# Kernel optimization log

Measured on AMD Instinct MI355X. Metric: run time of the kernel, lower is better.

Reference implementation:

```python
import jax, jax.numpy as jnp
import numpy as np

V, E = 100000, 128
B, Q, D = 512, 32, 256
K_NUM, SIGMA, EXACT_SIGMA = 21, 0.1, 0.001
EPS = 1e-8


def _kernel_params():
    # faithful to source (including the sigma/exact_sigma swap at the call site)
    l_mu = [1.0]
    bin_size = 2.0 / (K_NUM - 1)
    l_mu.append(1 - bin_size / 2)
    for j in range(1, K_NUM - 1):
        l_mu.append(l_mu[j] - bin_size)
    mus = sorted(l_mu)
    # kernel_sigmas(n, sigma=exact_sigma, exact_sigma=sigma) due to swapped call
    sig_list = [SIGMA] + [EXACT_SIGMA] * (K_NUM - 1)
    sigmas = sorted(sig_list)[::-1]
    return (jnp.asarray(mus, dtype=jnp.float32),
            jnp.asarray(sigmas, dtype=jnp.float32))

MUS, SIGMAS = _kernel_params()


def setup_inputs() -> dict:
    key = jax.random.key(0)
    ks = jax.random.split(key, 11)
    emb = jax.random.normal(ks[0], (V, E), dtype=jnp.float32)
    emb = emb.at[0].set(0.0)  # padding_idx=0
    w1 = jax.random.normal(ks[1], (K_NUM, 10), dtype=jnp.float32) / np.sqrt(K_NUM)
    b1 = jax.random.normal(ks[2], (10,), dtype=jnp.float32) * 0.01
    w2 = jax.random.normal(ks[3], (10, 5), dtype=jnp.float32) / np.sqrt(10)
    b2 = jax.random.normal(ks[4], (5,), dtype=jnp.float32) * 0.01
    w3 = jax.random.normal(ks[5], (5, 1), dtype=jnp.float32) / np.sqrt(5)
    b3 = jax.random.normal(ks[6], (1,), dtype=jnp.float32) * 0.01
    query1 = jax.random.randint(ks[7], (B, Q), 0, V, dtype=jnp.int64 if jax.config.jax_enable_x64 else jnp.int32)
    doc1 = jax.random.randint(ks[8], (B, D), 0, V, dtype=query1.dtype)
    query2 = jax.random.randint(ks[9], (B, Q), 0, V, dtype=query1.dtype)
    doc2 = jax.random.randint(ks[10], (B, D), 0, V, dtype=query1.dtype)
    return {"emb": emb, "w1": w1, "b1": b1, "w2": w2, "b2": b2,
            "w3": w3, "b3": b3, "query1": query1, "doc1": doc1,
            "query2": query2, "doc2": doc2}


def _l2norm(x):
    n = jnp.linalg.norm(x, axis=-1, keepdims=True)
    return x / jnp.maximum(n, EPS)


def _predict(emb, w1, b1, w2, b2, w3, b3, q_idx, d_idx):
    q_idx = jnp.clip(q_idx, 0, V - 1)
    d_idx = jnp.clip(d_idx, 0, V - 1)
    qn = _l2norm(emb[q_idx])            # [B,Q,E]
    dn = _l2norm(emb[d_idx])            # [B,D,E]
    mm = jnp.einsum('bqe,bde->bqd', qn, dn)  # cosine matching matrix [B,Q,D]
    # soft-histogram Gaussian kernel pooling: [B,Q,D,K]
    phi = jnp.exp(-0.5 * (mm[..., None] - MUS) ** 2 / SIGMAS ** 2)
    k_out = jnp.log1p(phi.sum(axis=2)).sum(axis=1)  # [B,K]
    x = jax.nn.relu(k_out) @ w1 + b1
    x = jax.nn.relu(x) @ w2 + b2
    x = jax.nn.relu(x) @ w3 + b3
    return x  # [B,1]


def reference(emb, w1, b1, w2, b2, w3, b3, query1, doc1, query2, doc2):
    logits_1 = _predict(emb, w1, b1, w2, b2, w3, b3, query1, doc1)
    logits_2 = _predict(emb, w1, b1, w2, b2, w3, b3, query2, doc2)
    return jax.nn.sigmoid(logits_1 - logits_2)
```

## Files before the change

### kernel.cpp

```cpp
#include <hip/hip_runtime.h>
#include <math.h>

#define V_SIZE 100000
#define E_DIM  128
#define B_SIZE 512
#define Q_LEN  32
#define D_LEN  256
#define K_NUM  21
#define ASTR   136


typedef _Float16 half8_t __attribute__((ext_vector_type(8)));
typedef float    float4_t __attribute__((ext_vector_type(4)));

__global__ __launch_bounds__(256, 4) void knrm_main(
    const float* __restrict__ emb,
    const int* __restrict__ q1, const int* __restrict__ d1,
    const int* __restrict__ q2, const int* __restrict__ d2,
    const float* __restrict__ w1, const float* __restrict__ b1,
    const float* __restrict__ w2, const float* __restrict__ b2,
    const float* __restrict__ w3, const float* __restrict__ b3,
    float* __restrict__ logits)
{
    const int b    = blockIdx.x;
    const int pair = blockIdx.y;
    const int t    = threadIdx.x;
    const int* __restrict__ qidx = pair ? q2 : q1;
    const int* __restrict__ didx = pair ? d2 : d1;

    __shared__ __align__(16) _Float16 Ah[Q_LEN * ASTR];
    __shared__ __align__(16) _Float16 Al[Q_LEN * ASTR];
    __shared__ __align__(16) _Float16 Bh[32 * ASTR];
    __shared__ __align__(16) _Float16 Bl[32 * ASTR];
    __shared__ float rnq[Q_LEN];
    __shared__ float rnd_s[32];
    __shared__ float phis[Q_LEN][22];
    __shared__ float ko[K_NUM];

    const int lane = t & 63;
    const int w    = t >> 6;
    const int quad = lane >> 4;
    const int l15  = lane & 15;
    const int qt   = w >> 1;
    const int dt   = w & 1;

    for (int i = t; i < Q_LEN * 22; i += 256) ((float*)phis)[i] = 0.f;

    const int drow = t >> 3;
    const int dcol = (t & 7) * 4;
    int dix[8];
    #pragma unroll
    for (int c = 0; c < 8; ++c) {
        int di = didx[b * D_LEN + c * 32 + drow];
        dix[c] = min(max(di, 0), V_SIZE - 1);
    }
    float4 pref[4];
    {
        const float4* dr = (const float4*)(emb + (size_t)dix[0] * E_DIM) + dcol;
        pref[0] = dr[0]; pref[1] = dr[1]; pref[2] = dr[2]; pref[3] = dr[3];
    }

    {
        const int qr = t >> 3;
        const int qc = t & 7;
        int qi = qidx[b * Q_LEN + qr];
        qi = min(max(qi, 0), V_SIZE - 1);
        const float4* src = (const float4*)(emb + (size_t)qi * E_DIM) + qc * 4;
        float4 v0 = src[0], v1 = src[1], v2 = src[2], v3 = src[3];
        float fv[16] = {v0.x,v0.y,v0.z,v0.w, v1.x,v1.y,v1.z,v1.w,
                        v2.x,v2.y,v2.z,v2.w, v3.x,v3.y,v3.z,v3.w};
        float ss = 0.f;
        half8_t h0, h1, l0, l1;
        #pragma unroll
        for (int j = 0; j < 8; ++j) {
            ss = fmaf(fv[j], fv[j], ss);
            _Float16 h = (_Float16)fv[j];
            h0[j] = h; l0[j] = (_Float16)(fv[j] - (float)h);
        }
        #pragma unroll
        for (int j = 0; j < 8; ++j) {
            ss = fmaf(fv[8 + j], fv[8 + j], ss);
            _Float16 h = (_Float16)fv[8 + j];
            h1[j] = h; l1[j] = (_Float16)(fv[8 + j] - (float)h);
        }
        *(half8_t*)&Ah[qr * ASTR + qc * 16]     = h0;
        *(half8_t*)&Ah[qr * ASTR + qc * 16 + 8] = h1;
        *(half8_t*)&Al[qr * ASTR + qc * 16]     = l0;
        *(half8_t*)&Al[qr * ASTR + qc * 16 + 8] = l1;
        ss += __shfl_xor(ss, 1, 8);
        ss += __shfl_xor(ss, 2, 8);
        ss += __shfl_xor(ss, 4, 8);
        if (qc == 0) rnq[qr] = 1.0f / fmaxf(sqrtf(ss), 1e-8f);
    }
    __syncthreads();

    float rnq4[4];
    #pragma unroll
    for (int r = 0; r < 4; ++r) rnq4[r] = rnq[qt * 16 + quad * 4 + r];

    const float cc0 = -0.5f / (0.1f * 0.1f);
    const float ccs = -0.5f / (0.001f * 0.001f);
    float breg[4] = {0.f, 0.f, 0.f, 0.f};

    for (int c = 0; c < 8; ++c) {
        {
            float fv[16] = {pref[0].x,pref[0].y,pref[0].z,pref[0].w,
                            pref[1].x,pref[1].y,pref[1].z,pref[1].w,
                            pref[2].x,pref[2].y,pref[2].z,pref[2].w,
                            pref[3].x,pref[3].y,pref[3].z,pref[3].w};
            float ss = 0.f;
            half8_t h0, h1, l0, l1;
            #pragma unroll
            for (int j = 0; j < 8; ++j) {
                ss = fmaf(fv[j], fv[j], ss);
                _Float16 h = (_Float16)fv[j];
                h0[j] = h; l0[j] = (_Float16)(fv[j] - (float)h);
            }
            #pragma unroll
            for (int j = 0; j < 8; ++j) {
                ss = fmaf(fv[8 + j], fv[8 + j], ss);
                _Float16 h = (_Float16)fv[8 + j];
                h1[j] = h; l1[j] = (_Float16)(fv[8 + j] - (float)h);
            }
            const int co = (t & 7) * 16;
            *(half8_t*)&Bh[drow * ASTR + co]     = h0;
            *(half8_t*)&Bh[drow * ASTR + co + 8] = h1;
            *(half8_t*)&Bl[drow * ASTR + co]     = l0;
            *(half8_t*)&Bl[drow * ASTR + co + 8] = l1;
            ss += __shfl_xor(ss, 1, 8);
            ss += __shfl_xor(ss, 2, 8);
            ss += __shfl_xor(ss, 4, 8);
            if ((t & 7) == 0) rnd_s[drow] = 1.0f / fmaxf(sqrtf(ss), 1e-8f);
        }
        __syncthreads();

        if (c < 7) {
            const float4* dr = (const float4*)(emb + (size_t)dix[c + 1] * E_DIM) + dcol;
            pref[0] = dr[0]; pref[1] = dr[1]; pref[2] = dr[2]; pref[3] = dr[3];
        }

        float4_t acc = {0.f, 0.f, 0.f, 0.f};
        const int arow = (qt * 16 + l15) * ASTR;
        const int brow = (dt * 16 + l15) * ASTR;
        #pragma unroll
        for (int s = 0; s < 4; ++s) {
            const int kof = s * 32 + quad * 8;
            half8_t ah = *(const half8_t*)&Ah[arow + kof];
            half8_t al = *(const half8_t*)&Al[arow + kof];
            half8_t bh = *(const half8_t*)&Bh[brow + kof];
            half8_t bl = *(const half8_t*)&Bl[brow + kof];
            acc = __builtin_amdgcn_mfma_f32_16x16x32_f16(ah, bh, acc, 0, 0, 0);
            acc = __builtin_amdgcn_mfma_f32_16x16x32_f16(ah, bl, acc, 0, 0, 0);
            acc = __builtin_amdgcn_mfma_f32_16x16x32_f16(al, bh, acc, 0, 0, 0);
        }

        const float rdv = rnd_s[dt * 16 + l15];
        #pragma unroll
        for (int r = 0; r < 4; ++r) {
            const float mm = acc[r] * rnq4[r] * rdv;
            const float x0 = mm + 0.95f;
            breg[r] += __expf(x0 * x0 * cc0);
            float g = rintf((mm + 0.85f) * 10.f);
            g = fminf(fmaxf(g, 0.f), 18.f);
            float mu = fmaf(g, 0.1f, -0.85f);
            int ks = (int)g + 1;
            if (mm > 0.975f) { mu = 1.0f; ks = 20; }
            const float xs = mm - mu;
            const float es = __expf(xs * xs * ccs);
            if (es > 0.f) atomicAdd(&phis[qt * 16 + quad * 4 + r][ks], es);
        }
        __syncthreads();
    }

    #pragma unroll
    for (int r = 0; r < 4; ++r) {
        float v = breg[r];
        v += __shfl_xor(v, 1, 16);
        v += __shfl_xor(v, 2, 16);
        v += __shfl_xor(v, 4, 16);
        v += __shfl_xor(v, 8, 16);
        if (l15 == 0) atomicAdd(&phis[qt * 16 + quad * 4 + r][0], v);
    }
    __syncthreads();

    for (int p = t; p < K_NUM * Q_LEN; p += 256) {
        const int q = p & 31;
        const int k = p >> 5;
        float l = log1pf(phis[q][k]);
        l += __shfl_xor(l, 1, 32);
        l += __shfl_xor(l, 2, 32);
        l += __shfl_xor(l, 4, 32);
        l += __shfl_xor(l, 8, 32);
        l += __shfl_xor(l, 16, 32);
        if (q == 0) ko[k] = l;
    }
    __syncthreads();

    if (t == 0) {
        float x1v[10];
        #pragma unroll
        for (int i = 0; i < 10; ++i) {
            float s = b1[i];
            for (int k = 0; k < K_NUM; ++k) {
                float v = ko[k] > 0.f ? ko[k] : 0.f;
                s = fmaf(v, w1[k * 10 + i], s);
            }
            x1v[i] = s;
        }
        float x2v[5];
        #pragma unroll
        for (int i = 0; i < 5; ++i) {
            float s = b2[i];
            #pragma unroll
            for (int k = 0; k < 10; ++k) {
                float v = x1v[k] > 0.f ? x1v[k] : 0.f;
                s = fmaf(v, w2[k * 5 + i], s);
            }
            x2v[i] = s;
        }
        float s3 = b3[0];
        #pragma unroll
        for (int k = 0; k < 5; ++k) {
            float v = x2v[k] > 0.f ? x2v[k] : 0.f;
            s3 = fmaf(v, w3[k], s3);
        }
        logits[pair * B_SIZE + b] = s3;
    }
}

__global__ void knrm_final(const float* __restrict__ logits, float* __restrict__ out)
{
    const int b = blockIdx.x * blockDim.x + threadIdx.x;
    if (b < B_SIZE) {
        const float dl = logits[b] - logits[B_SIZE + b];
        out[b] = 1.0f / (1.0f + __expf(-dl));
    }
}

extern "C" void kernel_launch(void* const* d_in, const int* in_sizes, int n_in,
                              void* d_out, int out_size, void* d_ws, size_t ws_size,
                              hipStream_t stream)
{
    const float* emb = (const float*)d_in[0];
    const float* w1  = (const float*)d_in[1];
    const float* b1  = (const float*)d_in[2];
    const float* w2  = (const float*)d_in[3];
    const float* b2  = (const float*)d_in[4];
    const float* w3  = (const float*)d_in[5];
    const float* b3  = (const float*)d_in[6];
    const int*   q1  = (const int*)d_in[7];
    const int*   d1  = (const int*)d_in[8];
    const int*   q2  = (const int*)d_in[9];
    const int*   d2  = (const int*)d_in[10];

    float* logits = (float*)d_ws;
    float* out    = (float*)d_out;

    dim3 grid(B_SIZE, 2);
    knrm_main<<<grid, 256, 0, stream>>>(emb, q1, d1, q2, d2,
                                        w1, b1, w2, b2, w3, b3, logits);
    knrm_final<<<(B_SIZE + 255) / 256, 256, 0, stream>>>(logits, out);
}
```

Before: 129.9 us.

## Load doc fragments straight into MFMA registers and drop per-chunk block barriers

```diff
diff --git a/kernel.cpp b/kernel.cpp
--- a/kernel.cpp
+++ b/kernel.cpp
@@ -7,10 +7,9 @@
 #define Q_LEN  32
 #define D_LEN  256
 #define K_NUM  21
-#define ASTR   136
-
-
-typedef _Float16 half8_t __attribute__((ext_vector_type(8)));
+
+
+typedef _Float16 half8_t  __attribute__((ext_vector_type(8)));
 typedef float    float4_t __attribute__((ext_vector_type(4)));
 
 __global__ __launch_bounds__(256, 4) void knrm_main(
@@ -28,12 +27,9 @@
     const int* __restrict__ qidx = pair ? q2 : q1;
     const int* __restrict__ didx = pair ? d2 : d1;
 
-    __shared__ __align__(16) _Float16 Ah[Q_LEN * ASTR];
-    __shared__ __align__(16) _Float16 Al[Q_LEN * ASTR];
-    __shared__ __align__(16) _Float16 Bh[32 * ASTR];
-    __shared__ __align__(16) _Float16 Bl[32 * ASTR];
+    __shared__ half8_t AfH[2][4][64];
+    __shared__ half8_t AfL[2][4][64];
     __shared__ float rnq[Q_LEN];
-    __shared__ float rnd_s[32];
     __shared__ float phis[Q_LEN][22];
     __shared__ float ko[K_NUM];
 
@@ -41,24 +37,8 @@
     const int w    = t >> 6;
     const int quad = lane >> 4;
     const int l15  = lane & 15;
-    const int qt   = w >> 1;
-    const int dt   = w & 1;
 
     for (int i = t; i < Q_LEN * 22; i += 256) ((float*)phis)[i] = 0.f;
-
-    const int drow = t >> 3;
-    const int dcol = (t & 7) * 4;
-    int dix[8];
-    #pragma unroll
-    for (int c = 0; c < 8; ++c) {
-        int di = didx[b * D_LEN + c * 32 + drow];
-        dix[c] = min(max(di, 0), V_SIZE - 1);
-    }
-    float4 pref[4];
-    {
-        const float4* dr = (const float4*)(emb + (size_t)dix[0] * E_DIM) + dcol;
-        pref[0] = dr[0]; pref[1] = dr[1]; pref[2] = dr[2]; pref[3] = dr[3];
-    }
 
     {
         const int qr = t >> 3;
@@ -83,10 +63,14 @@
             _Float16 h = (_Float16)fv[8 + j];
             h1[j] = h; l1[j] = (_Float16)(fv[8 + j] - (float)h);
         }
-        *(half8_t*)&Ah[qr * ASTR + qc * 16]     = h0;
-        *(half8_t*)&Ah[qr * ASTR + qc * 16 + 8] = h1;
-        *(half8_t*)&Al[qr * ASTR + qc * 16]     = l0;
-        *(half8_t*)&Al[qr * ASTR + qc * 16 + 8] = l1;
+        const int qt  = qr >> 4;
+        const int lr  = qr & 15;
+        const int s   = qc >> 1;
+        const int qd0 = (qc & 1) * 2;
+        AfH[qt][s][qd0 * 16 + lr]       = h0;
+        AfH[qt][s][(qd0 + 1) * 16 + lr] = h1;
+        AfL[qt][s][qd0 * 16 + lr]       = l0;
+        AfL[qt][s][(qd0 + 1) * 16 + lr] = l1;
         ss += __shfl_xor(ss, 1, 8);
         ss += __shfl_xor(ss, 2, 8);
         ss += __shfl_xor(ss, 4, 8);
@@ -94,92 +78,104 @@
     }
     __syncthreads();
 
-    float rnq4[4];
-    #pragma unroll
-    for (int r = 0; r < 4; ++r) rnq4[r] = rnq[qt * 16 + quad * 4 + r];
+    float rnqv[8];
+    #pragma unroll
+    for (int i = 0; i < 8; ++i) rnqv[i] = rnq[(i >> 2) * 16 + quad * 4 + (i & 3)];
 
     const float cc0 = -0.5f / (0.1f * 0.1f);
     const float ccs = -0.5f / (0.001f * 0.001f);
-    float breg[4] = {0.f, 0.f, 0.f, 0.f};
-
-    for (int c = 0; c < 8; ++c) {
-        {
-            float fv[16] = {pref[0].x,pref[0].y,pref[0].z,pref[0].w,
-                            pref[1].x,pref[1].y,pref[1].z,pref[1].w,
-                            pref[2].x,pref[2].y,pref[2].z,pref[2].w,
-                            pref[3].x,pref[3].y,pref[3].z,pref[3].w};
-            float ss = 0.f;
-            half8_t h0, h1, l0, l1;
+    float breg[8] = {0.f,0.f,0.f,0.f,0.f,0.f,0.f,0.f};
+
+    int dix[4];
+    #pragma unroll
+    for (int c = 0; c < 4; ++c) {
+        int di = didx[b * D_LEN + w * 64 + c * 16 + l15];
+        dix[c] = min(max(di, 0), V_SIZE - 1);
+    }
+
+    half8_t bh[4], bl[4];
+    float rnd;
+
+    auto convert = [&](const float4* v) {
+        float ss = 0.f;
+        #pragma unroll
+        for (int s = 0; s < 4; ++s) {
+            float f[8] = {v[2*s].x, v[2*s].y, v[2*s].z, v[2*s].w,
+                          v[2*s+1].x, v[2*s+1].y, v[2*s+1].z, v[2*s+1].w};
+            half8_t h, l;
             #pragma unroll
             for (int j = 0; j < 8; ++j) {
-                ss = fmaf(fv[j], fv[j], ss);
-                _Float16 h = (_Float16)fv[j];
-                h0[j] = h; l0[j] = (_Float16)(fv[j] - (float)h);
-            }
-            #pragma unroll
-            for (int j = 0; j < 8; ++j) {
-                ss = fmaf(fv[8 + j], fv[8 + j], ss);
-                _Float16 h = (_Float16)fv[8 + j];
-                h1[j] = h; l1[j] = (_Float16)(fv[8 + j] - (float)h);
-            }
-            const int co = (t & 7) * 16;
-            *(half8_t*)&Bh[drow * ASTR + co]     = h0;
-            *(half8_t*)&Bh[drow * ASTR + co + 8] = h1;
-            *(half8_t*)&Bl[drow * ASTR + co]     = l0;
-            *(half8_t*)&Bl[drow * ASTR + co + 8] = l1;
-            ss += __shfl_xor(ss, 1, 8);
-            ss += __shfl_xor(ss, 2, 8);
-            ss += __shfl_xor(ss, 4, 8);
-            if ((t & 7) == 0) rnd_s[drow] = 1.0f / fmaxf(sqrtf(ss), 1e-8f);
-        }
-        __syncthreads();
-
-        if (c < 7) {
-            const float4* dr = (const float4*)(emb + (size_t)dix[c + 1] * E_DIM) + dcol;
-            pref[0] = dr[0]; pref[1] = dr[1]; pref[2] = dr[2]; pref[3] = dr[3];
-        }
-
-        float4_t acc = {0.f, 0.f, 0.f, 0.f};
-        const int arow = (qt * 16 + l15) * ASTR;
-        const int brow = (dt * 16 + l15) * ASTR;
+                ss = fmaf(f[j], f[j], ss);
+                _Float16 hh = (_Float16)f[j];
+                h[j] = hh; l[j] = (_Float16)(f[j] - (float)hh);
+            }
+            bh[s] = h; bl[s] = l;
+        }
+        ss += __shfl_xor(ss, 16);
+        ss += __shfl_xor(ss, 32);
+        rnd = 1.0f / fmaxf(sqrtf(ss), 1e-8f);
+    };
+
+    {
+        const float4* dr = (const float4*)(emb + (size_t)dix[0] * E_DIM) + quad * 2;
+        float4 cur[8];
+        #pragma unroll
+        for (int s = 0; s < 4; ++s) { cur[2*s] = dr[s*8]; cur[2*s+1] = dr[s*8+1]; }
+        convert(cur);
+    }
+
+    #pragma unroll
+    for (int c = 0; c < 4; ++c) {
+        float4 nx[8];
+        if (c < 3) {
+            const float4* dr = (const float4*)(emb + (size_t)dix[c+1] * E_DIM) + quad * 2;
+            #pragma unroll
+            for (int s = 0; s < 4; ++s) { nx[2*s] = dr[s*8]; nx[2*s+1] = dr[s*8+1]; }
+        }
+
+        float4_t acc0 = {0.f,0.f,0.f,0.f}, acc1 = {0.f,0.f,0.f,0.f};
         #pragma unroll
         for (int s = 0; s < 4; ++s) {
-            const int kof = s * 32 + quad * 8;
-            half8_t ah = *(const half8_t*)&Ah[arow + kof];
-            half8_t al = *(const half8_t*)&Al[arow + kof];
-            half8_t bh = *(const half8_t*)&Bh[brow + kof];
-            half8_t bl = *(const half8_t*)&Bl[brow + kof];
-            acc = __builtin_amdgcn_mfma_f32_16x16x32_f16(ah, bh, acc, 0, 0, 0);
-            acc = __builtin_amdgcn_mfma_f32_16x16x32_f16(ah, bl, acc, 0, 0, 0);
-            acc = __builtin_amdgcn_mfma_f32_16x16x32_f16(al, bh, acc, 0, 0, 0);
-        }
-
-        const float rdv = rnd_s[dt * 16 + l15];
-        #pragma unroll
-        for (int r = 0; r < 4; ++r) {
-            const float mm = acc[r] * rnq4[r] * rdv;
-            const float x0 = mm + 0.95f;
-            breg[r] += __expf(x0 * x0 * cc0);
-            float g = rintf((mm + 0.85f) * 10.f);
-            g = fminf(fmaxf(g, 0.f), 18.f);
-            float mu = fmaf(g, 0.1f, -0.85f);
-            int ks = (int)g + 1;
-            if (mm > 0.975f) { mu = 1.0f; ks = 20; }
-            const float xs = mm - mu;
-            const float es = __expf(xs * xs * ccs);
-            if (es > 0.f) atomicAdd(&phis[qt * 16 + quad * 4 + r][ks], es);
-        }
-        __syncthreads();
-    }
-
-    #pragma unroll
-    for (int r = 0; r < 4; ++r) {
-        float v = breg[r];
+            half8_t a0h = AfH[0][s][lane], a0l = AfL[0][s][lane];
+            half8_t a1h = AfH[1][s][lane], a1l = AfL[1][s][lane];
+            acc0 = __builtin_amdgcn_mfma_f32_16x16x32_f16(a0h, bh[s], acc0, 0, 0, 0);
+            acc1 = __builtin_amdgcn_mfma_f32_16x16x32_f16(a1h, bh[s], acc1, 0, 0, 0);
+            acc0 = __builtin_amdgcn_mfma_f32_16x16x32_f16(a0l, bh[s], acc0, 0, 0, 0);
+            acc1 = __builtin_amdgcn_mfma_f32_16x16x32_f16(a1l, bh[s], acc1, 0, 0, 0);
+            acc0 = __builtin_amdgcn_mfma_f32_16x16x32_f16(a0h, bl[s], acc0, 0, 0, 0);
+            acc1 = __builtin_amdgcn_mfma_f32_16x16x32_f16(a1h, bl[s], acc1, 0, 0, 0);
+        }
+
+        #pragma unroll
+        for (int qt = 0; qt < 2; ++qt) {
+            const float4_t acc = qt ? acc1 : acc0;
+            #pragma unroll
+            for (int r = 0; r < 4; ++r) {
+                const float mm = acc[r] * rnqv[qt*4 + r] * rnd;
+                const float x0 = mm + 0.95f;
+                breg[qt*4 + r] += __expf(x0 * x0 * cc0);
+                float g = rintf((mm + 0.85f) * 10.f);
+                g = fminf(fmaxf(g, 0.f), 18.f);
+                float mu = fmaf(g, 0.1f, -0.85f);
+                int ks = (int)g + 1;
+                if (mm > 0.975f) { mu = 1.0f; ks = 20; }
+                const float xs = mm - mu;
+                const float es = __expf(xs * xs * ccs);
+                if (es > 0.f) atomicAdd(&phis[qt*16 + quad*4 + r][ks], es);
+            }
+        }
+
+        if (c < 3) convert(nx);
+    }
+
+    #pragma unroll
+    for (int i = 0; i < 8; ++i) {
+        float v = breg[i];
         v += __shfl_xor(v, 1, 16);
         v += __shfl_xor(v, 2, 16);
         v += __shfl_xor(v, 4, 16);
         v += __shfl_xor(v, 8, 16);
-        if (l15 == 0) atomicAdd(&phis[qt * 16 + quad * 4 + r][0], v);
+        if (l15 == 0) atomicAdd(&phis[(i >> 2) * 16 + quad * 4 + (i & 3)][0], v);
     }
     __syncthreads();
 
```

Result: faster. 124.7 us (-3.9%).
